# Performance work log

Measured on AMD Instinct MI355X. Metric: run time of the kernel, lower is better.

The kernel has to match this reference:

```python
import jax, jax.numpy as jnp
import numpy as np

NCLS, NDF, B = 256, 512, 1024
ALP = 0.1


def setup_inputs() -> dict:
    key = jax.random.key(0)
    k1, k2, k3 = jax.random.split(key, 3)
    df = jax.random.normal(k1, (B, NDF), dtype=jnp.float32)
    gt = jax.random.randint(k2, (B,), 0, NCLS)
    fc = jax.random.normal(k3, (NCLS, NDF), dtype=jnp.float32)
    return {"df": df, "gt": gt, "fc": fc}


def _update_stats(df, gt):
    """Sequential per-sample running mean/var update (moving_avg=False branch).
    Faithful to the torch no_grad loop: per-class counter `it`, c1=it/(it+1),
    c2=1/(it+1); mean[t]=f when it==0 else mean[t]*c1+f*c2;
    var[t]=var[t]*c1 + (f-mean[t])**2 * c1*c2. Buffers start at zero.
    """
    mean0 = jnp.zeros((NCLS, NDF), jnp.float32)
    var0 = jnp.zeros((NCLS, NDF), jnp.float32)
    it0 = jnp.zeros((NCLS,), jnp.int32)

    def step(carry, xt):
        mean, var, it = carry
        f, t = xt
        n = it[t]
        nf = n.astype(jnp.float32)
        c1 = nf / (nf + 1.0)
        c2 = 1.0 / (nf + 1.0)
        m_t = jnp.where(n == 0, f, mean[t] * c1 + f * c2)
        a = (f - m_t) ** 2
        v_t = var[t] * c1 + a * c1 * c2
        return (mean.at[t].set(m_t), var.at[t].set(v_t), it.at[t].add(1)), None

    (mean, var, it), _ = jax.lax.scan(step, (mean0, var0, it0), (df, gt))
    return mean, var


def reference(df, gt, fc):
    # stats updated from detached features (torch uses no_grad)
    _, var = _update_stats(jax.lax.stop_gradient(df), gt)
    Var = var[gt]          # (B, ndf)
    Fc = fc[gt]            # (B, ndf): column of fc for each sample's class
    W = fc[None, :, :] - Fc[:, None, :]  # (B, ncls, ndf)
    # score[b,c] = W[b,c,:].df[b,:] + alp/2 * (W**2)[b,c,:].Var[b,:]
    score = jnp.einsum('bcd,bd->bc', W, df) \
        + 0.5 * ALP * jnp.einsum('bcd,bd->bc', W * W, Var)
    return score[:, :, None]  # (B, ncls, 1), matching torch matmul output
```

## Files before the change

### kernel.cpp

```cpp
#include <hip/hip_runtime.h>

#define NCLS 256
#define NDF  512
#define BSZ  1024
#define ALP  0.1f
#define LSTR 68


__device__ __forceinline__ void gemm_inner(const float (*As)[LSTR], const float (*Bs)[LSTR],
                                           int tx, int ty, float4* acc) {
#pragma unroll
    for (int kk = 0; kk < 32; ++kk) {
        const float4 a = *(const float4*)&As[kk][ty * 4];
        const float4 b = *(const float4*)&Bs[kk][tx * 4];
        acc[0].x += a.x * b.x; acc[0].y += a.x * b.y; acc[0].z += a.x * b.z; acc[0].w += a.x * b.w;
        acc[1].x += a.y * b.x; acc[1].y += a.y * b.y; acc[1].z += a.y * b.z; acc[1].w += a.y * b.w;
        acc[2].x += a.z * b.x; acc[2].y += a.z * b.y; acc[2].z += a.z * b.z; acc[2].w += a.z * b.w;
        acc[3].x += a.w * b.x; acc[3].y += a.w * b.y; acc[3].z += a.w * b.z; acc[3].w += a.w * b.w;
    }
}

__global__ __launch_bounds__(256) void fused_main(const float* __restrict__ df,
                                                  const int* __restrict__ gt,
                                                  const float* __restrict__ fc,
                                                  float* __restrict__ s1p,
                                                  float* __restrict__ Rp) {
    __shared__ float As[32][LSTR];
    __shared__ float Bs[32][LSTR];
    __shared__ int gts[BSZ];
    __shared__ unsigned long long bmap[64 * 16];

    const int tid = threadIdx.x;
    const int bid = blockIdx.x;
    const int tx = tid & 15, ty = tid >> 4;

    float4 acc[4];
    acc[0] = make_float4(0.f, 0.f, 0.f, 0.f);
    acc[1] = acc[0]; acc[2] = acc[0]; acc[3] = acc[0];

    if (bid < 256) {
        const int z = bid & 3;
        const int tile = bid >> 2;
        const int bm = tile & 15, bn = tile >> 4;
        const int arow = tid >> 2;
        const int kq = (tid & 3) << 3;
        const float* Ag = df + (bm * 64 + arow) * NDF + z * 128 + kq;
        const float* Bg = fc + (bn * 64 + arow) * NDF + z * 128 + kq;

        float4 a0 = *(const float4*)Ag, a1 = *(const float4*)(Ag + 4);
        float4 b0 = *(const float4*)Bg, b1 = *(const float4*)(Bg + 4);
#pragma unroll 1
        for (int ks = 0; ks < 4; ++ks) {
            __syncthreads();
            As[kq + 0][arow] = a0.x; As[kq + 1][arow] = a0.y; As[kq + 2][arow] = a0.z; As[kq + 3][arow] = a0.w;
            As[kq + 4][arow] = a1.x; As[kq + 5][arow] = a1.y; As[kq + 6][arow] = a1.z; As[kq + 7][arow] = a1.w;
            Bs[kq + 0][arow] = b0.x; Bs[kq + 1][arow] = b0.y; Bs[kq + 2][arow] = b0.z; Bs[kq + 3][arow] = b0.w;
            Bs[kq + 4][arow] = b1.x; Bs[kq + 5][arow] = b1.y; Bs[kq + 6][arow] = b1.z; Bs[kq + 7][arow] = b1.w;
            __syncthreads();
            if (ks < 3) {
                const int off = (ks + 1) * 32;
                a0 = *(const float4*)(Ag + off); a1 = *(const float4*)(Ag + off + 4);
                b0 = *(const float4*)(Bg + off); b1 = *(const float4*)(Bg + off + 4);
            }
            gemm_inner(As, Bs, tx, ty, acc);
        }
        float* Cp = s1p + z * (BSZ * NCLS) + (bm * 64 + ty * 4) * NCLS + bn * 64 + tx * 4;
#pragma unroll
        for (int i = 0; i < 4; ++i) *(float4*)(Cp + i * NCLS) = acc[i];
    } else {
        const int r = bid - 256;
        const int z = r & 7;
        const int tile = r >> 3;
        const int bm = tile & 3, bn = tile >> 2;
        const int D0 = z * 64;
        const int clocal = tid >> 2;
        const int dg = tid & 3;
        const int myclass = bm * 64 + clocal;
        const int dim0 = D0 + dg * 16;

        for (int i = tid; i < BSZ; i += 256) gts[i] = gt[i];
        for (int i = tid; i < 1024; i += 256) bmap[i] = 0ull;
        __syncthreads();
        for (int i = tid; i < BSZ; i += 256) {
            const int c = gts[i] - bm * 64;
            if ((unsigned)c < 64u) atomicOr(&bmap[c * 16 + (i >> 6)], 1ull << (i & 63));
        }
        const float* fct = fc + myclass * NDF + dim0;
        float fcq[16];
        {
            const float4 q0 = ((const float4*)fct)[0], q1 = ((const float4*)fct)[1];
            const float4 q2 = ((const float4*)fct)[2], q3 = ((const float4*)fct)[3];
            fcq[0]=q0.x; fcq[1]=q0.y; fcq[2]=q0.z; fcq[3]=q0.w;
            fcq[4]=q1.x; fcq[5]=q1.y; fcq[6]=q1.z; fcq[7]=q1.w;
            fcq[8]=q2.x; fcq[9]=q2.y; fcq[10]=q2.z; fcq[11]=q2.w;
            fcq[12]=q3.x; fcq[13]=q3.y; fcq[14]=q3.z; fcq[15]=q3.w;
        }
        __syncthreads();

        float m[16], v[16];
#pragma unroll
        for (int j = 0; j < 16; ++j) { m[j] = 0.f; v[j] = 0.f; }
        float nf = 0.f;
        {
            int w = 0;
            unsigned long long bits = bmap[clocal * 16];
            auto next = [&]() -> int {
                while (bits == 0ull) {
                    if (w >= 15) return -1;
                    bits = bmap[clocal * 16 + (++w)];
                }
                const int b = __ffsll((unsigned long long)bits) - 1;
                bits &= bits - 1ull;
                return (w << 6) + b;
            };
            int cur = next();
            float f[16];
            if (cur >= 0) {
                const float* p = df + cur * NDF + dim0;
                const float4 q0 = ((const float4*)p)[0], q1 = ((const float4*)p)[1];
                const float4 q2 = ((const float4*)p)[2], q3 = ((const float4*)p)[3];
                f[0]=q0.x; f[1]=q0.y; f[2]=q0.z; f[3]=q0.w;
                f[4]=q1.x; f[5]=q1.y; f[6]=q1.z; f[7]=q1.w;
                f[8]=q2.x; f[9]=q2.y; f[10]=q2.z; f[11]=q2.w;
                f[12]=q3.x; f[13]=q3.y; f[14]=q3.z; f[15]=q3.w;
            }
            while (cur >= 0) {
                const int nxt = next();
                float g[16];
                if (nxt >= 0) {
                    const float* p = df + nxt * NDF + dim0;
                    const float4 q0 = ((const float4*)p)[0], q1 = ((const float4*)p)[1];
                    const float4 q2 = ((const float4*)p)[2], q3 = ((const float4*)p)[3];
                    g[0]=q0.x; g[1]=q0.y; g[2]=q0.z; g[3]=q0.w;
                    g[4]=q1.x; g[5]=q1.y; g[6]=q1.z; g[7]=q1.w;
                    g[8]=q2.x; g[9]=q2.y; g[10]=q2.z; g[11]=q2.w;
                    g[12]=q3.x; g[13]=q3.y; g[14]=q3.z; g[15]=q3.w;
                }
                const float c2 = 1.0f / (nf + 1.0f);
                const float c1 = nf * c2;
                const float c12 = c1 * c2;
#pragma unroll
                for (int j = 0; j < 16; ++j) {
                    m[j] = m[j] * c1 + f[j] * c2;
                    const float a = f[j] - m[j];
                    v[j] = v[j] * c1 + a * a * c12;
                }
                nf += 1.0f;
#pragma unroll
                for (int j = 0; j < 16; ++j) f[j] = g[j];
                cur = nxt;
            }
        }

        const int crow = tid >> 2, kq = (tid & 3) << 3;
        const float* Bg = fc + (bn * 64 + crow) * NDF + D0;
        float4 b0 = *(const float4*)(Bg + kq), b1 = *(const float4*)(Bg + kq + 4);
#pragma unroll 1
        for (int ks = 0; ks < 4; ++ks) {
            const bool quad = (ks >= 2);
            float4 w0 = b0, w1 = b1;
            if (quad) {
                w0.x *= w0.x; w0.y *= w0.y; w0.z *= w0.z; w0.w *= w0.w;
                w1.x *= w1.x; w1.y *= w1.y; w1.z *= w1.z; w1.w *= w1.w;
            }
            __syncthreads();
            if ((dg >> 1) == (ks & 1)) {
                const int kb = (dg & 1) * 16;
#pragma unroll
                for (int j = 0; j < 16; ++j) {
                    As[kb + j][clocal] = quad ? v[j] : (-2.f * fcq[j] * v[j]);
                }
            }
            Bs[kq + 0][crow] = w0.x; Bs[kq + 1][crow] = w0.y; Bs[kq + 2][crow] = w0.z; Bs[kq + 3][crow] = w0.w;
            Bs[kq + 4][crow] = w1.x; Bs[kq + 5][crow] = w1.y; Bs[kq + 6][crow] = w1.z; Bs[kq + 7][crow] = w1.w;
            __syncthreads();
            if (ks < 3) {
                const int off = ((ks + 1) & 1) * 32;
                b0 = *(const float4*)(Bg + off + kq);
                b1 = *(const float4*)(Bg + off + kq + 4);
            }
            gemm_inner(As, Bs, tx, ty, acc);
        }
        float* Cp = Rp + z * (NCLS * NCLS) + (bm * 64 + ty * 4) * NCLS + bn * 64 + tx * 4;
#pragma unroll
        for (int i = 0; i < 4; ++i) *(float4*)(Cp + i * NCLS) = acc[i];
    }
}

__global__ __launch_bounds__(256) void epilogue_kernel(const float* __restrict__ s1p,
                                                       const float* __restrict__ Rp,
                                                       const int* __restrict__ gt,
                                                       float* __restrict__ out) {
    __shared__ float sv1[NCLS];
    __shared__ float svR[NCLS];
    const int b = blockIdx.x;
    const int c = threadIdx.x;
    const int t = gt[b];
    float v1 = 0.f;
#pragma unroll
    for (int zz = 0; zz < 4; ++zz) v1 += s1p[zz * (BSZ * NCLS) + b * NCLS + c];
    float vR = 0.f;
#pragma unroll
    for (int zz = 0; zz < 8; ++zz) vR += Rp[zz * (NCLS * NCLS) + t * NCLS + c];
    sv1[c] = v1;
    svR[c] = vR;
    __syncthreads();
    out[b * NCLS + c] = (v1 - sv1[t]) + 0.5f * ALP * (vR - svR[t]);
}

extern "C" void kernel_launch(void* const* d_in, const int* in_sizes, int n_in,
                              void* d_out, int out_size, void* d_ws, size_t ws_size,
                              hipStream_t stream) {
    const float* df = (const float*)d_in[0];
    const int* gt = (const int*)d_in[1];
    const float* fc = (const float*)d_in[2];
    float* out = (float*)d_out;

    float* ws = (float*)d_ws;
    float* s1p = ws;
    float* Rp = s1p + 4 * BSZ * NCLS;

    fused_main<<<384, 256, 0, stream>>>(df, gt, fc, s1p, Rp);
    epilogue_kernel<<<BSZ, 256, 0, stream>>>(s1p, Rp, gt, out);
}
```

Measured before the change: 29.64 us.

## Use bf16 MFMA for both GEMM paths and vectorize the epilogue

Replaces the FP32 register-blocked FMA GEMM in both block roles with bf16 MFMA 16x16x32 instructions. Operands are converted to bf16 with round-to-nearest-even and staged in XOR-swizzled LDS tiles. The epilogue now handles four samples per block with float4 loads and drops the shared-memory exchange. This cuts ALU time in the small GEMMs at the cost of bf16 precision, which raises the error in the score outputs.

```diff
diff --git a/kernel.cpp b/kernel.cpp
--- a/kernel.cpp
+++ b/kernel.cpp
@@ -4,20 +4,23 @@
 #define NDF  512
 #define BSZ  1024
 #define ALP  0.1f
-#define LSTR 68
-
-
-__device__ __forceinline__ void gemm_inner(const float (*As)[LSTR], const float (*Bs)[LSTR],
-                                           int tx, int ty, float4* acc) {
-#pragma unroll
-    for (int kk = 0; kk < 32; ++kk) {
-        const float4 a = *(const float4*)&As[kk][ty * 4];
-        const float4 b = *(const float4*)&Bs[kk][tx * 4];
-        acc[0].x += a.x * b.x; acc[0].y += a.x * b.y; acc[0].z += a.x * b.z; acc[0].w += a.x * b.w;
-        acc[1].x += a.y * b.x; acc[1].y += a.y * b.y; acc[1].z += a.y * b.z; acc[1].w += a.y * b.w;
-        acc[2].x += a.z * b.x; acc[2].y += a.z * b.y; acc[2].z += a.z * b.z; acc[2].w += a.z * b.w;
-        acc[3].x += a.w * b.x; acc[3].y += a.w * b.y; acc[3].z += a.w * b.z; acc[3].w += a.w * b.w;
-    }
+
+
+typedef __attribute__((ext_vector_type(8))) short bf16x8;
+typedef __attribute__((ext_vector_type(4))) float f32x4;
+
+__device__ __forceinline__ unsigned rne_pk(float lo, float hi) {
+    union { float f; unsigned u; } a, b;
+    a.f = lo; b.f = hi;
+    unsigned ua = (a.u + 0x7FFFu + ((a.u >> 16) & 1u)) >> 16;
+    unsigned ub = (b.u + 0x7FFFu + ((b.u >> 16) & 1u)) & 0xFFFF0000u;
+    return ua | ub;
+}
+__device__ __forceinline__ uint4 pk16(float4 p, float4 q) {
+    uint4 r;
+    r.x = rne_pk(p.x, p.y); r.y = rne_pk(p.z, p.w);
+    r.z = rne_pk(q.x, q.y); r.w = rne_pk(q.z, q.w);
+    return r;
 }
 
 __global__ __launch_bounds__(256) void fused_main(const float* __restrict__ df,
@@ -25,58 +28,94 @@
                                                   const float* __restrict__ fc,
                                                   float* __restrict__ s1p,
                                                   float* __restrict__ Rp) {
-    __shared__ float As[32][LSTR];
-    __shared__ float Bs[32][LSTR];
+    __shared__ alignas(16) char Asb[64 * 128];
+    __shared__ alignas(16) char Bsb[64 * 128];
     __shared__ int gts[BSZ];
     __shared__ unsigned long long bmap[64 * 16];
 
     const int tid = threadIdx.x;
     const int bid = blockIdx.x;
-    const int tx = tid & 15, ty = tid >> 4;
-
-    float4 acc[4];
-    acc[0] = make_float4(0.f, 0.f, 0.f, 0.f);
-    acc[1] = acc[0]; acc[2] = acc[0]; acc[3] = acc[0];
+    const int lane = tid & 63;
+    const int wv = tid >> 6;
+    const int wm = (wv >> 1) * 32, wn = (wv & 1) * 32;
+    const int fr = lane & 15;
+    const int fkb = (lane >> 4) * 16;
+    const int fswz = (fr & 7) << 4;
+
+    const int sr = tid >> 2;
+    const int skb = (tid & 3) * 32;
+    const int sswz = (sr & 7) << 4;
+    char* arow = Asb + sr * 128;
+    char* brow = Bsb + sr * 128;
+
+    f32x4 acc[2][2];
+    acc[0][0] = 0.f; acc[0][1] = 0.f; acc[1][0] = 0.f; acc[1][1] = 0.f;
+
+    auto mma_step = [&](int k0b) {
+        const int kb = (k0b + fkb) ^ fswz;
+        const bf16x8 aF0 = *(const bf16x8*)(Asb + (wm + fr) * 128 + kb);
+        const bf16x8 aF1 = *(const bf16x8*)(Asb + (wm + 16 + fr) * 128 + kb);
+        const bf16x8 bF0 = *(const bf16x8*)(Bsb + (wn + fr) * 128 + kb);
+        const bf16x8 bF1 = *(const bf16x8*)(Bsb + (wn + 16 + fr) * 128 + kb);
+        acc[0][0] = __builtin_amdgcn_mfma_f32_16x16x32_bf16(aF0, bF0, acc[0][0], 0, 0, 0);
+        acc[0][1] = __builtin_amdgcn_mfma_f32_16x16x32_bf16(aF0, bF1, acc[0][1], 0, 0, 0);
+        acc[1][0] = __builtin_amdgcn_mfma_f32_16x16x32_bf16(aF1, bF0, acc[1][0], 0, 0, 0);
+        acc[1][1] = __builtin_amdgcn_mfma_f32_16x16x32_bf16(aF1, bF1, acc[1][1], 0, 0, 0);
+    };
+    auto store_tile = [&](float* base) {
+#pragma unroll
+        for (int mi = 0; mi < 2; ++mi)
+#pragma unroll
+            for (int ni = 0; ni < 2; ++ni)
+#pragma unroll
+                for (int r2 = 0; r2 < 4; ++r2)
+                    base[(wm + mi * 16 + (lane >> 4) * 4 + r2) * NCLS + wn + ni * 16 + fr] =
+                        acc[mi][ni][r2];
+    };
 
     if (bid < 256) {
         const int z = bid & 3;
         const int tile = bid >> 2;
         const int bm = tile & 15, bn = tile >> 4;
-        const int arow = tid >> 2;
-        const int kq = (tid & 3) << 3;
-        const float* Ag = df + (bm * 64 + arow) * NDF + z * 128 + kq;
-        const float* Bg = fc + (bn * 64 + arow) * NDF + z * 128 + kq;
-
-        float4 a0 = *(const float4*)Ag, a1 = *(const float4*)(Ag + 4);
-        float4 b0 = *(const float4*)Bg, b1 = *(const float4*)(Bg + 4);
-#pragma unroll 1
-        for (int ks = 0; ks < 4; ++ks) {
-            __syncthreads();
-            As[kq + 0][arow] = a0.x; As[kq + 1][arow] = a0.y; As[kq + 2][arow] = a0.z; As[kq + 3][arow] = a0.w;
-            As[kq + 4][arow] = a1.x; As[kq + 5][arow] = a1.y; As[kq + 6][arow] = a1.z; As[kq + 7][arow] = a1.w;
-            Bs[kq + 0][arow] = b0.x; Bs[kq + 1][arow] = b0.y; Bs[kq + 2][arow] = b0.z; Bs[kq + 3][arow] = b0.w;
-            Bs[kq + 4][arow] = b1.x; Bs[kq + 5][arow] = b1.y; Bs[kq + 6][arow] = b1.z; Bs[kq + 7][arow] = b1.w;
-            __syncthreads();
-            if (ks < 3) {
-                const int off = (ks + 1) * 32;
-                a0 = *(const float4*)(Ag + off); a1 = *(const float4*)(Ag + off + 4);
-                b0 = *(const float4*)(Bg + off); b1 = *(const float4*)(Bg + off + 4);
-            }
-            gemm_inner(As, Bs, tx, ty, acc);
-        }
-        float* Cp = s1p + z * (BSZ * NCLS) + (bm * 64 + ty * 4) * NCLS + bn * 64 + tx * 4;
-#pragma unroll
-        for (int i = 0; i < 4; ++i) *(float4*)(Cp + i * NCLS) = acc[i];
+        const float* Ag = df + (bm * 64 + sr) * NDF + z * 128 + (tid & 3) * 16;
+        const float* Bg = fc + (bn * 64 + sr) * NDF + z * 128 + (tid & 3) * 16;
+
+        float4 a0 = ((const float4*)Ag)[0], a1 = ((const float4*)Ag)[1],
+               a2 = ((const float4*)Ag)[2], a3 = ((const float4*)Ag)[3];
+        float4 b0 = ((const float4*)Bg)[0], b1 = ((const float4*)Bg)[1],
+               b2 = ((const float4*)Bg)[2], b3 = ((const float4*)Bg)[3];
+        *(uint4*)(arow + (skb ^ sswz)) = pk16(a0, a1);
+        *(uint4*)(arow + ((skb + 16) ^ sswz)) = pk16(a2, a3);
+        *(uint4*)(brow + (skb ^ sswz)) = pk16(b0, b1);
+        *(uint4*)(brow + ((skb + 16) ^ sswz)) = pk16(b2, b3);
+        __syncthreads();
+        a0 = ((const float4*)(Ag + 64))[0]; a1 = ((const float4*)(Ag + 64))[1];
+        a2 = ((const float4*)(Ag + 64))[2]; a3 = ((const float4*)(Ag + 64))[3];
+        b0 = ((const float4*)(Bg + 64))[0]; b1 = ((const float4*)(Bg + 64))[1];
+        b2 = ((const float4*)(Bg + 64))[2]; b3 = ((const float4*)(Bg + 64))[3];
+        mma_step(0); mma_step(64);
+        __syncthreads();
+        *(uint4*)(arow + (skb ^ sswz)) = pk16(a0, a1);
+        *(uint4*)(arow + ((skb + 16) ^ sswz)) = pk16(a2, a3);
+        *(uint4*)(brow + (skb ^ sswz)) = pk16(b0, b1);
+        *(uint4*)(brow + ((skb + 16) ^ sswz)) = pk16(b2, b3);
+        __syncthreads();
+        mma_step(0); mma_step(64);
+        store_tile(s1p + z * (BSZ * NCLS) + (bm * 64) * NCLS + bn * 64);
     } else {
         const int r = bid - 256;
         const int z = r & 7;
         const int tile = r >> 3;
         const int bm = tile & 3, bn = tile >> 2;
         const int D0 = z * 64;
-        const int clocal = tid >> 2;
+        const int clocal = sr;
         const int dg = tid & 3;
         const int myclass = bm * 64 + clocal;
         const int dim0 = D0 + dg * 16;
+
+        const float* Bg = fc + (bn * 64 + sr) * NDF + D0 + (tid & 3) * 16;
+        const float4 b0 = ((const float4*)Bg)[0], b1 = ((const float4*)Bg)[1],
+                     b2 = ((const float4*)Bg)[2], b3 = ((const float4*)Bg)[3];
 
         for (int i = tid; i < BSZ; i += 256) gts[i] = gt[i];
         for (int i = tid; i < 1024; i += 256) bmap[i] = 0ull;
@@ -152,38 +191,38 @@
             }
         }
 
-        const int crow = tid >> 2, kq = (tid & 3) << 3;
-        const float* Bg = fc + (bn * 64 + crow) * NDF + D0;
-        float4 b0 = *(const float4*)(Bg + kq), b1 = *(const float4*)(Bg + kq + 4);
-#pragma unroll 1
-        for (int ks = 0; ks < 4; ++ks) {
-            const bool quad = (ks >= 2);
-            float4 w0 = b0, w1 = b1;
-            if (quad) {
-                w0.x *= w0.x; w0.y *= w0.y; w0.z *= w0.z; w0.w *= w0.w;
-                w1.x *= w1.x; w1.y *= w1.y; w1.z *= w1.z; w1.w *= w1.w;
-            }
-            __syncthreads();
-            if ((dg >> 1) == (ks & 1)) {
-                const int kb = (dg & 1) * 16;
-#pragma unroll
-                for (int j = 0; j < 16; ++j) {
-                    As[kb + j][clocal] = quad ? v[j] : (-2.f * fcq[j] * v[j]);
-                }
-            }
-            Bs[kq + 0][crow] = w0.x; Bs[kq + 1][crow] = w0.y; Bs[kq + 2][crow] = w0.z; Bs[kq + 3][crow] = w0.w;
-            Bs[kq + 4][crow] = w1.x; Bs[kq + 5][crow] = w1.y; Bs[kq + 6][crow] = w1.z; Bs[kq + 7][crow] = w1.w;
-            __syncthreads();
-            if (ks < 3) {
-                const int off = ((ks + 1) & 1) * 32;
-                b0 = *(const float4*)(Bg + off + kq);
-                b1 = *(const float4*)(Bg + off + kq + 4);
-            }
-            gemm_inner(As, Bs, tx, ty, acc);
-        }
-        float* Cp = Rp + z * (NCLS * NCLS) + (bm * 64 + ty * 4) * NCLS + bn * 64 + tx * 4;
-#pragma unroll
-        for (int i = 0; i < 4; ++i) *(float4*)(Cp + i * NCLS) = acc[i];
+        {
+            float4 p0, p1, p2, p3;
+            p0.x=-2.f*fcq[0]*v[0];  p0.y=-2.f*fcq[1]*v[1];  p0.z=-2.f*fcq[2]*v[2];  p0.w=-2.f*fcq[3]*v[3];
+            p1.x=-2.f*fcq[4]*v[4];  p1.y=-2.f*fcq[5]*v[5];  p1.z=-2.f*fcq[6]*v[6];  p1.w=-2.f*fcq[7]*v[7];
+            p2.x=-2.f*fcq[8]*v[8];  p2.y=-2.f*fcq[9]*v[9];  p2.z=-2.f*fcq[10]*v[10]; p2.w=-2.f*fcq[11]*v[11];
+            p3.x=-2.f*fcq[12]*v[12]; p3.y=-2.f*fcq[13]*v[13]; p3.z=-2.f*fcq[14]*v[14]; p3.w=-2.f*fcq[15]*v[15];
+            *(uint4*)(arow + (skb ^ sswz)) = pk16(p0, p1);
+            *(uint4*)(arow + ((skb + 16) ^ sswz)) = pk16(p2, p3);
+            *(uint4*)(brow + (skb ^ sswz)) = pk16(b0, b1);
+            *(uint4*)(brow + ((skb + 16) ^ sswz)) = pk16(b2, b3);
+        }
+        __syncthreads();
+        mma_step(0); mma_step(64);
+        __syncthreads();
+        {
+            float4 p0, p1, p2, p3, s0, s1, s2, s3;
+            p0.x=v[0];  p0.y=v[1];  p0.z=v[2];  p0.w=v[3];
+            p1.x=v[4];  p1.y=v[5];  p1.z=v[6];  p1.w=v[7];
+            p2.x=v[8];  p2.y=v[9];  p2.z=v[10]; p2.w=v[11];
+            p3.x=v[12]; p3.y=v[13]; p3.z=v[14]; p3.w=v[15];
+            s0.x=b0.x*b0.x; s0.y=b0.y*b0.y; s0.z=b0.z*b0.z; s0.w=b0.w*b0.w;
+            s1.x=b1.x*b1.x; s1.y=b1.y*b1.y; s1.z=b1.z*b1.z; s1.w=b1.w*b1.w;
+            s2.x=b2.x*b2.x; s2.y=b2.y*b2.y; s2.z=b2.z*b2.z; s2.w=b2.w*b2.w;
+            s3.x=b3.x*b3.x; s3.y=b3.y*b3.y; s3.z=b3.z*b3.z; s3.w=b3.w*b3.w;
+            *(uint4*)(arow + (skb ^ sswz)) = pk16(p0, p1);
+            *(uint4*)(arow + ((skb + 16) ^ sswz)) = pk16(p2, p3);
+            *(uint4*)(brow + (skb ^ sswz)) = pk16(s0, s1);
+            *(uint4*)(brow + ((skb + 16) ^ sswz)) = pk16(s2, s3);
+        }
+        __syncthreads();
+        mma_step(0); mma_step(64);
+        store_tile(Rp + z * (NCLS * NCLS) + (bm * 64) * NCLS + bn * 64);
     }
 }
 
@@ -191,21 +230,33 @@
                                                        const float* __restrict__ Rp,
                                                        const int* __restrict__ gt,
                                                        float* __restrict__ out) {
-    __shared__ float sv1[NCLS];
-    __shared__ float svR[NCLS];
-    const int b = blockIdx.x;
-    const int c = threadIdx.x;
+    const int b = blockIdx.x * 4 + (threadIdx.x >> 6);
+    const int cq = (threadIdx.x & 63) * 4;
     const int t = gt[b];
-    float v1 = 0.f;
-#pragma unroll
-    for (int zz = 0; zz < 4; ++zz) v1 += s1p[zz * (BSZ * NCLS) + b * NCLS + c];
-    float vR = 0.f;
-#pragma unroll
-    for (int zz = 0; zz < 8; ++zz) vR += Rp[zz * (NCLS * NCLS) + t * NCLS + c];
-    sv1[c] = v1;
-    svR[c] = vR;
-    __syncthreads();
-    out[b * NCLS + c] = (v1 - sv1[t]) + 0.5f * ALP * (vR - svR[t]);
+    float4 v1 = make_float4(0.f, 0.f, 0.f, 0.f);
+    float v1t = 0.f;
+#pragma unroll
+    for (int zz = 0; zz < 4; ++zz) {
+        const float* row = s1p + zz * (BSZ * NCLS) + b * NCLS;
+        const float4 q = *(const float4*)(row + cq);
+        v1.x += q.x; v1.y += q.y; v1.z += q.z; v1.w += q.w;
+        v1t += row[t];
+    }
+    float4 vR = make_float4(0.f, 0.f, 0.f, 0.f);
+    float vRt = 0.f;
+#pragma unroll
+    for (int zz = 0; zz < 8; ++zz) {
+        const float* row = Rp + zz * (NCLS * NCLS) + t * NCLS;
+        const float4 q = *(const float4*)(row + cq);
+        vR.x += q.x; vR.y += q.y; vR.z += q.z; vR.w += q.w;
+        vRt += row[t];
+    }
+    float4 o;
+    o.x = (v1.x - v1t) + 0.5f * ALP * (vR.x - vRt);
+    o.y = (v1.y - v1t) + 0.5f * ALP * (vR.y - vRt);
+    o.z = (v1.z - v1t) + 0.5f * ALP * (vR.z - vRt);
+    o.w = (v1.w - v1t) + 0.5f * ALP * (vR.w - vRt);
+    *(float4*)(out + b * NCLS + cq) = o;
 }
 
 extern "C" void kernel_launch(void* const* d_in, const int* in_sizes, int n_in,
@@ -221,5 +272,5 @@
     float* Rp = s1p + 4 * BSZ * NCLS;
 
     fused_main<<<384, 256, 0, stream>>>(df, gt, fc, s1p, Rp);
-    epilogue_kernel<<<BSZ, 256, 0, stream>>>(s1p, Rp, gt, out);
-}
+    epilogue_kernel<<<256, 256, 0, stream>>>(s1p, Rp, gt, out);
+}
```

Result: faster. 25.10 us (-15.3%).
